# Optimization experiments

Measured on AMD Instinct MI355X. Metric: run time of the kernel, lower is better.

Reference implementation:

```python
import jax, jax.numpy as jnp
import numpy as np
from jax.scipy.special import erf

# module constants (init kwargs)
BOX = 128
RES = 1.0
EPS_IN = 6.5
EPS_OUT = 79.0
ION_SIZE = 1.0
WAT_SIZE = 1.4
ASIGMA = 2.0
KAPPA02 = 0.106
CHARGE_CONV = 7046.52
WR = 8       # splat window radius in voxels ~ ceil(R_max + probe + d*asigma)
N_ITER = 30  # Jacobi iterations for the linearized PB solve


def setup_inputs():
    key = jax.random.key(0)
    kc, kq, kr, kn = jax.random.split(key, 4)
    B, N = 2, 1024
    lo, hi = 0.2 * BOX * RES, 0.8 * BOX * RES
    coords = jax.random.uniform(kc, (B, 3 * N), dtype=jnp.float32, minval=lo, maxval=hi)
    charges = 0.5 * jax.random.normal(kq, (B, N), dtype=jnp.float32)
    radii = jax.random.uniform(kr, (B, N), dtype=jnp.float32, minval=1.0, maxval=2.0)
    assigned_params = jnp.stack([charges, radii], axis=-1)  # [B,N,2] = (charge, radius)
    num_atoms = jax.random.randint(kn, (B,), N // 2, N + 1, dtype=jnp.int32)
    return {"coords": coords, "assigned_params": assigned_params, "num_atoms": num_atoms}


def _flat_scatter_add(vals, idx, B):
    # idx [...,3] int32 clipped voxel indices; vals same leading shape; batched scatter-add
    flat = (idx[..., 0] * BOX + idx[..., 1]) * BOX + idx[..., 2]
    flat = flat + (jnp.arange(B, dtype=jnp.int32) * (BOX ** 3)).reshape((B,) + (1,) * (flat.ndim - 1))
    acc = jnp.zeros((B * BOX ** 3,), vals.dtype).at[flat.reshape(-1)].add(vals.reshape(-1))
    return acc.reshape(B, BOX, BOX, BOX)


def _eps_channel(xyz, radii, atom_mask, offset, extra_r):
    # rho_sum(x) = prod_atoms (1 - smoothed_indicator); accumulated in log space via scatter-add
    o = jnp.arange(-WR, WR + 1, dtype=jnp.int32)
    offs = jnp.stack(jnp.meshgrid(o, o, o, indexing="ij"), axis=-1).reshape(-1, 3)  # [W3,3]
    idx0 = jnp.round(xyz / RES - offset).astype(jnp.int32)            # [B,N,3]
    idx = idx0[:, :, None, :] + offs[None, None]                      # [B,N,W3,3]
    pos = (idx.astype(xyz.dtype) + offset) * RES
    r = jnp.sqrt(jnp.sum((pos - xyz[:, :, None, :]) ** 2, axis=-1) + 1e-12)
    rho = 0.5 * (1.0 - erf((r - (radii[:, :, None] + extra_r)) / ASIGMA))
    logv = jnp.log1p(-jnp.clip(rho, 0.0, 1.0 - 1e-6))
    inb = jnp.all((idx >= 0) & (idx < BOX), axis=-1)
    logv = jnp.where(inb & atom_mask[:, :, None], logv, 0.0)
    acc = _flat_scatter_add(logv, jnp.clip(idx, 0, BOX - 1), xyz.shape[0])
    return jnp.exp(acc)


def _coords2q(xyz, charges, atom_mask):
    # trilinear charge spreading onto the voxel grid
    g = xyz / RES
    i0 = jnp.floor(g).astype(jnp.int32)
    f = g - i0.astype(g.dtype)
    c = jnp.stack(jnp.meshgrid(*([jnp.arange(2)] * 3), indexing="ij"), -1).reshape(-1, 3)  # [8,3]
    idx = i0[:, :, None, :] + c[None, None]                           # [B,N,8,3]
    w = jnp.prod(jnp.where(c[None, None].astype(bool), f[:, :, None, :], 1.0 - f[:, :, None, :]), axis=-1)
    vals = w * charges[:, :, None]
    inb = jnp.all((idx >= 0) & (idx < BOX), axis=-1)
    vals = jnp.where(inb & atom_mask[:, :, None], vals, 0.0)
    return _flat_scatter_add(vals, jnp.clip(idx, 0, BOX - 1), xyz.shape[0])


def _shift(a, axis, step):
    # out[i] = a[i+step], zero padded (Dirichlet phi=0 boundary)
    pad = [(0, 0)] * a.ndim
    sl = [slice(None)] * a.ndim
    if step == 1:
        pad[axis] = (0, 1); sl[axis] = slice(1, None)
    else:
        pad[axis] = (1, 0); sl[axis] = slice(0, -1)
    return jnp.pad(a, pad)[tuple(sl)]


def _qeps2phi(q, eps):
    # Jacobi iteration for div(eps grad phi) - kappa02*lambda*phi = -q on staggered eps grids
    ex, ey, ez, lmbd = eps[:, 0], eps[:, 1], eps[:, 2], eps[:, 3]
    exm, eym, ezm = _shift(ex, 1, -1), _shift(ey, 2, -1), _shift(ez, 3, -1)
    denom = ex + exm + ey + eym + ez + ezm + KAPPA02 * lmbd * RES ** 2
    rhs = q * RES ** 2
    def body(_, phi):
        num = (ex * _shift(phi, 1, 1) + exm * _shift(phi, 1, -1)
               + ey * _shift(phi, 2, 1) + eym * _shift(phi, 2, -1)
               + ez * _shift(phi, 3, 1) + ezm * _shift(phi, 3, -1) + rhs)
        return num / denom
    return jax.lax.fori_loop(0, N_ITER, body, jnp.zeros_like(q))


def reference(coords, assigned_params, num_atoms):
    B = coords.shape[0]
    N = coords.shape[1] // 3
    xyz = coords.reshape(B, N, 3)
    atom_mask = jnp.arange(N)[None, :] < num_atoms[:, None]
    charges, radii = assigned_params[..., 0], assigned_params[..., 1]
    # channels 0..2: face-staggered eps grids (water probe); channel 3: ion accessibility
    specs = [((0.5, 0.0, 0.0), WAT_SIZE), ((0.0, 0.5, 0.0), WAT_SIZE),
             ((0.0, 0.0, 0.5), WAT_SIZE), ((0.0, 0.0, 0.0), ION_SIZE)]
    rho = jnp.stack([_eps_channel(xyz, radii, atom_mask, jnp.asarray(off, xyz.dtype), er)
                     for off, er in specs], axis=1)  # [B,4,S,S,S]
    eps = jnp.concatenate([(1.0 - rho[:, :3]) * (EPS_IN - EPS_OUT) + EPS_OUT,
                           (1.0 - rho[:, 3:4])], axis=1)
    q = _coords2q(xyz, charges, atom_mask) * CHARGE_CONV
    phi = _qeps2phi(q, eps)
    return (q, eps, phi)
```

## Files before the change

### kernel.cpp

```cpp
#include <hip/hip_runtime.h>
#include <math.h>

#define BOX 128
#define MCELLS (BOX*BOX*BOX)
#define TABN 512
#define SATN 256
typedef unsigned short u16;

__device__ __forceinline__ float bf2f(u16 h) {
  union { unsigned u; float f; } c; c.u = ((unsigned)h) << 16; return c.f;
}
__device__ __forceinline__ u16 f2bf(float f) {
  union { float f; unsigned u; } c; c.f = f;
  unsigned r = c.u + 0x7FFF + ((c.u >> 16) & 1);
  return (u16)(r >> 16);
}
__device__ __forceinline__ unsigned pk2(float a, float b) {
  return (unsigned)f2bf(a) | ((unsigned)f2bf(b) << 16);
}
__device__ __forceinline__ float plo(unsigned p) {
  union { unsigned u; float f; } c; c.u = p << 16; return c.f;
}
__device__ __forceinline__ float phh(unsigned p) {
  union { unsigned u; float f; } c; c.u = p & 0xFFFF0000u; return c.f;
}
__device__ __forceinline__ void up8(uint4 p, float* o) {
  o[0] = plo(p.x); o[1] = phh(p.x); o[2] = plo(p.y); o[3] = phh(p.y);
  o[4] = plo(p.z); o[5] = phh(p.z); o[6] = plo(p.w); o[7] = phh(p.w);
}
__device__ __forceinline__ uint4 pk8(const float* o) {
  return make_uint4(pk2(o[0], o[1]), pk2(o[2], o[3]),
                    pk2(o[4], o[5]), pk2(o[6], o[7]));
}

__device__ __forceinline__ float f_exact(float u) {
  float au = fabsf(u);
  float tt = __builtin_amdgcn_rcpf(fmaf(0.3275911f, au, 1.0f));
  float poly = tt * fmaf(tt, fmaf(tt, fmaf(tt, fmaf(tt, 1.061405429f,
                   -1.453152027f), 1.421413741f), -0.284496736f),
                   0.254829592f);
  float e = fmaf(-poly, __expf(-u * u), 1.0f);
  float erfu = (u < 0.0f) ? -e : e;
  float s = fmaf(0.5f, erfu, 0.5f);
  s = fminf(fmaxf(s, 1e-6f), 1.0f);
  return __logf(s);
}

__device__ __forceinline__ float tlookf(const float2* __restrict__ ftab,
                                        float r2, float aoff, float hidu) {
  float r = __builtin_amdgcn_sqrtf(r2);
  float t = fmaf(r, hidu, aoff);
  t = fminf(fmaxf(t, 0.0f), 511.75f);
  int j = (int)t;
  float fr = t - (float)j;
  float2 e = ftab[j];
  return fmaf(fr, e.y, e.x);
}

__global__ __launch_bounds__(256) void eps_gather_kernel(
    const float* __restrict__ coords, const float* __restrict__ params,
    const int* __restrict__ num_atoms, float* __restrict__ eps_out, int N) {
  __shared__ float4 satA[SATN];
  __shared__ float  satW[SATN];
  __shared__ float2 ftab[TABN];
  __shared__ int scnt;

  const int xt = blockIdx.x, yt = blockIdx.y;
  const int bz = blockIdx.z;
  const int b = bz >> 4, zt = bz & 15;
  const int tid = threadIdx.x;

  const float u0 = -1.8f;
  const float du = (2.2f - u0) / (float)TABN;
  const float inv_du = (float)TABN / (2.2f - u0);
  const float hidu = 0.5f * inv_du;
  const float dAI = 0.2f * inv_du;

  if (tid == 0) scnt = 0;
  __syncthreads();

  const float lox = (float)(xt * 8), hix = lox + 7.5f;
  const float loy = (float)(yt * 8), hiy = loy + 7.5f;
  const float loz = (float)(zt * 8), hiz = loz + 7.5f;

  const int na = num_atoms[b];
  for (int a = tid; a < N; a += 256) {
    if (a < na) {
      float ax = coords[(size_t)b * 3 * N + a * 3 + 0];
      float ay = coords[(size_t)b * 3 * N + a * 3 + 1];
      float az = coords[(size_t)b * 3 * N + a * 3 + 2];
      float rad = params[((size_t)b * N + a) * 2 + 1];
      float cx = fminf(fmaxf(ax, lox), hix);
      float cy = fminf(fmaxf(ay, loy), hiy);
      float cz = fminf(fmaxf(az, loz), hiz);
      float ddx = ax - cx, ddy = ay - cy, ddz = az - cz;
      float cut = rad + 5.85f;
      if (ddx * ddx + ddy * ddy + ddz * ddz < cut * cut) {
        int s = atomicAdd(&scnt, 1);
        if (s < SATN) {
          float Rw = rad + 1.4f;
          float cw = rad + 5.8f;
          satA[s] = make_float4(ax, ay, az, cw * cw);
          satW[s] = (1.8f - 0.5f * Rw) * inv_du;
        }
      }
    }
  }
  __syncthreads();
  const int cnt = min(scnt, SATN);

  const int zq = tid & 3, yy = (tid >> 2) & 7, xx = tid >> 5;
  const int xi = xt * 8 + xx, yi = yt * 8 + yy, zi = zt * 8 + zq * 2;
  const int v = (xi << 14) + (yi << 7) + zi;
  const size_t eb = (size_t)b * 4 * MCELLS;

  if (cnt == 0) {
    *(float2*)(eps_out + eb + 0 * MCELLS + v) = make_float2(79.0f, 79.0f);
    *(float2*)(eps_out + eb + 1 * MCELLS + v) = make_float2(79.0f, 79.0f);
    *(float2*)(eps_out + eb + 2 * MCELLS + v) = make_float2(79.0f, 79.0f);
    *(float2*)(eps_out + eb + (size_t)3 * MCELLS + v) = make_float2(0.0f, 0.0f);
    return;
  }

  for (int j = tid; j < TABN; j += 256) {
    float uj = fmaf(du, (float)j, u0);
    float f0 = f_exact(uj);
    float f1 = f_exact(uj + du);
    ftab[j] = (j == TABN - 1) ? make_float2(0.0f, 0.0f)
                              : make_float2(f0, f1 - f0);
  }
  __syncthreads();

  const float xf = (float)xi, yf = (float)yi, zf = (float)zi;
  float acc[4][2] = {{0.f, 0.f}, {0.f, 0.f}, {0.f, 0.f}, {0.f, 0.f}};

  for (int j = 0; j < cnt; ++j) {
    float4 A = satA[j];
    float aW = satW[j];
    float dx = xf - A.x, dy = yf - A.y, dzb = zf - A.z;
    float cw2 = A.w;

    float dx2 = dx * dx, dxh = dx + 0.5f, dxh2 = dxh * dxh;
    float dy2 = dy * dy, dyh = dy + 0.5f, dyh2 = dyh * dyh;
    float mdx = fminf(dx2, dxh2);
    float mdy = fminf(dy2, dyh2);
    float zhi = dzb + 1.5f;
    float mdz = (dzb > 0.f) ? dzb * dzb : (zhi < 0.f ? zhi * zhi : 0.f);
    if (mdx + mdy + mdz >= cw2) continue;

    float aI = aW + dAI;
    float sW0 = dxh2 + dy2, sW1 = dx2 + dyh2, sxy = dx2 + dy2;
#pragma unroll
    for (int k = 0; k < 2; ++k) {
      float dzv = dzb + (float)k;
      float dz2 = dzv * dzv, dzh = dzv + 0.5f, dzh2 = dzh * dzh;
      acc[0][k] += tlookf(ftab, sW0 + dz2, aW, hidu);
      acc[1][k] += tlookf(ftab, sW1 + dz2, aW, hidu);
      acc[2][k] += tlookf(ftab, sxy + dzh2, aW, hidu);
      acc[3][k] += tlookf(ftab, sxy + dz2, aI, hidu);
    }
  }

#pragma unroll
  for (int ch = 0; ch < 4; ++ch) {
    float e0 = __expf(acc[ch][0]), e1 = __expf(acc[ch][1]);
    float2 o = (ch < 3)
        ? make_float2(fmaf(72.5f, e0, 6.5f), fmaf(72.5f, e1, 6.5f))
        : make_float2(1.0f - e0, 1.0f - e1);
    *(float2*)(eps_out + eb + (size_t)ch * MCELLS + v) = o;
  }
}

__global__ __launch_bounds__(256) void q_scatter_kernel(
    const float* __restrict__ coords, const float* __restrict__ params,
    const int* __restrict__ num_atoms, float* __restrict__ q, int N, int B) {
  int t = blockIdx.x * blockDim.x + threadIdx.x;
  if (t >= B * N) return;
  int b = t / N, atom = t % N;
  if (atom >= num_atoms[b]) return;

  const float x = coords[(size_t)b * 3 * N + atom * 3 + 0];
  const float y = coords[(size_t)b * 3 * N + atom * 3 + 1];
  const float z = coords[(size_t)b * 3 * N + atom * 3 + 2];
  const float c = params[((size_t)b * N + atom) * 2 + 0] * 7046.52f;

  float fx0 = floorf(x), fy0 = floorf(y), fz0 = floorf(z);
  int ix = (int)fx0, iy = (int)fy0, iz = (int)fz0;
  float fx = x - fx0, fy = y - fy0, fz = z - fz0;

  float* __restrict__ g = q + (size_t)b * MCELLS;
  for (int k = 0; k < 8; ++k) {
    int cx = (k >> 2) & 1, cy = (k >> 1) & 1, cz = k & 1;
    int jx = ix + cx, jy = iy + cy, jz = iz + cz;
    if ((unsigned)jx >= (unsigned)BOX || (unsigned)jy >= (unsigned)BOX ||
        (unsigned)jz >= (unsigned)BOX) continue;
    float w = (cx ? fx : 1.0f - fx) * (cy ? fy : 1.0f - fy) *
              (cz ? fz : 1.0f - fz);
    atomicAdd(&g[(jx * BOX + jy) * BOX + jz], w * c);
  }
}

__global__ __launch_bounds__(256) void prep8_kernel(
    const float* __restrict__ eps, const float* __restrict__ q,
    u16* __restrict__ exb, u16* __restrict__ eyb, u16* __restrict__ ezb,
    u16* __restrict__ rdn, u16* __restrict__ rq2, u16* __restrict__ phiA,
    u16* __restrict__ pure16, int B) {
  const int per_b = MCELLS / 8;
  int t = blockIdx.x * 256 + threadIdx.x;
  if (t >= B * per_b) return;
  int b = t >> 18;
  int r = t & (per_b - 1);
  int zg = r & 15, y = (r >> 4) & 127, x = r >> 11;
  int z0 = zg << 3;
  int v = (x << 14) | (y << 7) | z0;
  size_t cell = (size_t)b * MCELLS + v;

  const float* ex = eps + (size_t)(b * 4 + 0) * MCELLS;
  const float* ey = eps + (size_t)(b * 4 + 1) * MCELLS;
  const float* ez = eps + (size_t)(b * 4 + 2) * MCELLS;
  const float* lm = eps + (size_t)(b * 4 + 3) * MCELLS;

  float exA[8], eyA[8], ezA9[9], lA[8], qA[8], xmA[8], ymA[8];
  *(float4*)(exA)     = *(const float4*)(ex + v);
  *(float4*)(exA + 4) = *(const float4*)(ex + v + 4);
  *(float4*)(eyA)     = *(const float4*)(ey + v);
  *(float4*)(eyA + 4) = *(const float4*)(ey + v + 4);
  *(float4*)(ezA9 + 1) = *(const float4*)(ez + v);
  *(float4*)(ezA9 + 5) = *(const float4*)(ez + v + 4);
  ezA9[0] = (z0 > 0) ? ez[v - 1] : 0.0f;
  *(float4*)(lA)     = *(const float4*)(lm + v);
  *(float4*)(lA + 4) = *(const float4*)(lm + v + 4);
  *(float4*)(qA)     = *(const float4*)(q + cell);
  *(float4*)(qA + 4) = *(const float4*)(q + cell + 4);
  if (x > 0) {
    *(float4*)(xmA)     = *(const float4*)(ex + v - 16384);
    *(float4*)(xmA + 4) = *(const float4*)(ex + v - 16384 + 4);
  } else {
#pragma unroll
    for (int i = 0; i < 8; ++i) xmA[i] = 0.0f;
  }
  if (y > 0) {
    *(float4*)(ymA)     = *(const float4*)(ey + v - 128);
    *(float4*)(ymA + 4) = *(const float4*)(ey + v - 128 + 4);
  } else {
#pragma unroll
    for (int i = 0; i < 8; ++i) ymA[i] = 0.0f;
  }

  float rdA[8], rqA[8];
  bool pu = true;
#pragma unroll
  for (int i = 0; i < 8; ++i) {
    float den = exA[i] + xmA[i] + eyA[i] + ymA[i] + ezA9[i + 1] + ezA9[i] +
                0.106f * lA[i];
    rdA[i] = __builtin_amdgcn_rcpf(den);
    rqA[i] = qA[i] * rdA[i];
    pu &= (exA[i] == 79.0f) & (eyA[i] == 79.0f) & (ezA9[i + 1] == 79.0f) &
          (lA[i] == 0.0f) & (qA[i] == 0.0f);
  }
  *(uint4*)(exb + cell) = pk8(exA);
  *(uint4*)(eyb + cell) = pk8(eyA);
  *(uint4*)(ezb + cell) = pk8(ezA9 + 1);
  *(uint4*)(rdn + cell) = pk8(rdA);
  uint4 rqp = pk8(rqA);
  *(uint4*)(rq2 + cell) = rqp;
  *(uint4*)(phiA + cell) = rqp;

  unsigned long long bal = __ballot(pu);
  int lane = threadIdx.x & 63;
  if ((lane & 15) == 0) {
    unsigned m = (unsigned)((bal >> (lane & 48)) & 0xFFFFull);
    pure16[((size_t)b << 14) + (x << 7) + y] = (u16)m;
  }
}

__global__ __launch_bounds__(256) void flag_kernel(
    const u16* __restrict__ pure16, unsigned char* __restrict__ flags,
    int B) {
  int t = blockIdx.x * 256 + threadIdx.x;
  if (t >= B * 128 * 32) return;
  int b = t >> 12;
  int r = t & 4095;
  int x = r >> 5, yq = r & 31;
  unsigned char f = 0;
  if (x > 0 && x < 127 && yq > 0 && yq < 31) {
    const u16* P = pure16 + ((size_t)b << 14);
    bool ok = true;
    int y0 = yq << 2;
    for (int dx = -1; dx <= 1; ++dx)
      for (int yy = y0 - 1; yy <= y0 + 4; ++yy)
        ok &= (P[(x + dx) * 128 + yy] == 0xFFFFu);
    f = ok ? 1 : 0;
  }
  flags[t] = f;
}

__device__ __forceinline__ void stage8(
    const u16* __restrict__ sp, int cst, int c0, int z0, size_t cell,
    int gx, int gy, bool bulk,
    const u16* __restrict__ exb, const u16* __restrict__ eyb,
    const u16* __restrict__ ezb, const u16* __restrict__ rdn,
    const u16* __restrict__ rq2, float* o) {
  const u16* pc0 = sp + (c0 << 7) + z0;
  uint4 pc = *(const uint4*)pc0;
  u16 zmu = (z0 > 0)   ? pc0[-1] : (u16)0;
  u16 zpu = (z0 < 120) ? pc0[8]  : (u16)0;
  uint4 xp = *(const uint4*)(pc0 + (cst << 7));
  uint4 xm = *(const uint4*)(pc0 - (cst << 7));
  uint4 yp = *(const uint4*)(pc0 + 128);
  uint4 ym = *(const uint4*)(pc0 - 128);

  float pz[10];
  pz[0] = bf2f(zmu); up8(pc, pz + 1); pz[9] = bf2f(zpu);
  float xpA[8], xmA[8], ypA[8], ymA[8];
  up8(xp, xpA); up8(xm, xmA); up8(yp, ypA); up8(ym, ymA);

  if (bulk) {
    float rdc  = bf2f(f2bf(__builtin_amdgcn_rcpf(474.0f)));
    float rdc0 = bf2f(f2bf(__builtin_amdgcn_rcpf(395.0f)));
#pragma unroll
    for (int i = 0; i < 8; ++i) {
      float s = xpA[i] + xmA[i] + ypA[i] + ymA[i] + pz[i] + pz[i + 2];
      float rd = (z0 + i == 0) ? rdc0 : rdc;
      o[i] = rd * (79.0f * s);
    }
  } else {
    const uint4 z4 = make_uint4(0, 0, 0, 0);
    uint4 ec  = *(const uint4*)(exb + cell);
    uint4 em  = (gx > 0) ? *(const uint4*)(exb + cell - 16384) : z4;
    uint4 yc  = *(const uint4*)(eyb + cell);
    uint4 ym4 = (gy > 0) ? *(const uint4*)(eyb + cell - 128) : z4;
    uint4 zc  = *(const uint4*)(ezb + cell);
    u16 ezm0  = (z0 > 0) ? ezb[cell - 1] : (u16)0;
    uint4 rd4 = *(const uint4*)(rdn + cell);
    uint4 rq4 = *(const uint4*)(rq2 + cell);
    float exA[8], exmA[8], eyA[8], eymA[8], ezA[9], rdA[8], rqA[8];
    up8(ec, exA); up8(em, exmA); up8(yc, eyA); up8(ym4, eymA);
    ezA[0] = bf2f(ezm0); up8(zc, ezA + 1);
    up8(rd4, rdA); up8(rq4, rqA);
#pragma unroll
    for (int i = 0; i < 8; ++i) {
      float num = exA[i] * xpA[i];
      num = fmaf(exmA[i], xmA[i], num);
      num = fmaf(eyA[i],  ypA[i], num);
      num = fmaf(eymA[i], ymA[i], num);
      num = fmaf(ezA[i + 1], pz[i + 2], num);
      num = fmaf(ezA[i],     pz[i],     num);
      o[i] = fmaf(rdA[i], num, rqA[i]);
    }
  }
}

__global__ __launch_bounds__(256, 4) void fused2_kernel(
    const u16* __restrict__ pin, u16* __restrict__ pout,
    const u16* __restrict__ exb, const u16* __restrict__ eyb,
    const u16* __restrict__ ezb, const u16* __restrict__ rdn,
    const u16* __restrict__ rq2, const u16* __restrict__ pure16) {
  __shared__ u16 s0[12 * 8 * 128];
  __shared__ u16 s1[10 * 6 * 128];
  __shared__ u16 sbulk16[96];

  const int flat = blockIdx.x;
  const int xcd = flat & 7;
  const int idx = flat >> 3;
  const int x0 = ((xcd << 1) | (idx & 1)) * 8;
  const int rem = idx >> 1;
  const int y0 = (rem & 31) * 4;
  const int b = rem >> 5;

  const int tid = threadIdx.x;
  const size_t bbase = (size_t)b << 21;
  const uint4 z4 = make_uint4(0, 0, 0, 0);

  if (tid < 96) {
    int cx = tid >> 3, cy = tid & 7;
    int gx = x0 - 2 + cx, gy = y0 - 2 + cy;
    unsigned sb = 0;
    if (gx >= 1 && gx <= 126 && gy >= 1 && gy <= 126) {
      const u16* P = pure16 + ((size_t)b << 14);
      sb = (unsigned)P[(gx << 7) + gy] & P[((gx - 1) << 7) + gy] &
           P[((gx + 1) << 7) + gy] & P[(gx << 7) + gy - 1] &
           P[(gx << 7) + gy + 1];
    }
    sbulk16[tid] = (u16)(sb & ((sb << 1) | 1u));
  }

  for (int i = tid; i < 96 * 16; i += 256) {
    int col = i >> 4, zc = i & 15;
    int cx = col >> 3, cy = col & 7;
    int gx = x0 - 2 + cx, gy = y0 - 2 + cy;
    uint4 vv = z4;
    if ((unsigned)gx < 128u && (unsigned)gy < 128u)
      vv = *(const uint4*)(pin + (bbase | (gx << 14) | (gy << 7) | (zc << 3)));
    ((uint4*)s0)[(col << 4) + zc] = vv;
  }
  __syncthreads();

  for (int u = tid; u < 60 * 16; u += 256) {
    int col = u >> 4, zc = u & 15, zz = zc << 3;
    int cx = col / 6, cy = col - cx * 6;
    int gx = x0 - 1 + cx, gy = y0 - 1 + cy;
    uint4* dst = (uint4*)(s1 + (col << 7) + zz);
    if ((unsigned)gx >= 128u || (unsigned)gy >= 128u) { *dst = z4; continue; }
    int c0 = (cx + 1) * 8 + (cy + 1);
    size_t cell = bbase | (gx << 14) | (gy << 7) | zz;
    float o[8];
    stage8(s0, 8, c0, zz, cell, gx, gy, ((sbulk16[c0] >> zc) & 1) != 0,
           exb, eyb, ezb, rdn, rq2, o);
    *dst = pk8(o);
  }
  __syncthreads();

  for (int u = tid; u < 32 * 16; u += 256) {
    int col = u >> 4, zc = u & 15, zz = zc << 3;
    int cx = col >> 2, cy = col & 3;
    int gx = x0 + cx, gy = y0 + cy;
    int c1 = (cx + 1) * 6 + (cy + 1);
    size_t cell = bbase | (gx << 14) | (gy << 7) | zz;
    float o[8];
    stage8(s1, 6, c1, zz, cell, gx, gy,
           ((sbulk16[(cx + 2) * 8 + (cy + 2)] >> zc) & 1) != 0,
           exb, eyb, ezb, rdn, rq2, o);
    *(uint4*)(pout + cell) = pk8(o);
  }
}

__global__ __launch_bounds__(256) void sweep_final_kernel(
    const u16* __restrict__ pin, float* __restrict__ poutf,
    const u16* __restrict__ exb, const u16* __restrict__ eyb,
    const u16* __restrict__ ezb, const u16* __restrict__ rdn,
    const u16* __restrict__ rq2, const unsigned char* __restrict__ flags,
    int units) {
  int t = blockIdx.x * 256 + threadIdx.x;
  if (t >= units) return;
  int b = t >> 18;
  int r = t & ((1 << 18) - 1);
  int zg = r & 15, y = (r >> 4) & 127, x = r >> 11;
  int z0 = zg << 3;
  int v = (x << 14) | (y << 7) | z0;
  size_t cell = (size_t)b * MCELLS + v;

  const uint4 z4 = make_uint4(0, 0, 0, 0);
  uint4 pc = *(const uint4*)(pin + cell);
  u16 zmu = (z0 > 0)   ? pin[cell - 1] : (u16)0;
  u16 zpu = (z0 < 120) ? pin[cell + 8] : (u16)0;
  uint4 xp = (x < 127) ? *(const uint4*)(pin + cell + 16384) : z4;
  uint4 xm = (x > 0)   ? *(const uint4*)(pin + cell - 16384) : z4;
  uint4 yp = (y < 127) ? *(const uint4*)(pin + cell + 128) : z4;
  uint4 ym = (y > 0)   ? *(const uint4*)(pin + cell - 128) : z4;

  float pz[10];
  pz[0] = bf2f(zmu); up8(pc, pz + 1); pz[9] = bf2f(zpu);
  float xpA[8], xmA[8], ypA[8], ymA[8];
  up8(xp, xpA); up8(xm, xmA); up8(yp, ypA); up8(ym, ymA);

  bool bulk = flags[(b << 12) + (x << 5) + (y >> 2)] != 0;

  float o[8];
  if (bulk) {
    float rdc  = bf2f(f2bf(__builtin_amdgcn_rcpf(474.0f)));
    float rdc0 = bf2f(f2bf(__builtin_amdgcn_rcpf(395.0f)));
#pragma unroll
    for (int i = 0; i < 8; ++i) {
      float s = xpA[i] + xmA[i] + ypA[i] + ymA[i] + pz[i] + pz[i + 2];
      float rd = (z0 + i == 0) ? rdc0 : rdc;
      o[i] = rd * (79.0f * s);
    }
  } else {
    uint4 ec  = *(const uint4*)(exb + cell);
    uint4 em  = (x > 0) ? *(const uint4*)(exb + cell - 16384) : z4;
    uint4 yc  = *(const uint4*)(eyb + cell);
    uint4 ym4 = (y > 0) ? *(const uint4*)(eyb + cell - 128) : z4;
    uint4 zc  = *(const uint4*)(ezb + cell);
    u16 ezm0  = (z0 > 0) ? ezb[cell - 1] : (u16)0;
    uint4 rd4 = *(const uint4*)(rdn + cell);
    uint4 rq4 = *(const uint4*)(rq2 + cell);
    float exA[8], exmA[8], eyA[8], eymA[8], ezA[9], rdA[8], rqA[8];
    up8(ec, exA); up8(em, exmA); up8(yc, eyA); up8(ym4, eymA);
    ezA[0] = bf2f(ezm0); up8(zc, ezA + 1);
    up8(rd4, rdA); up8(rq4, rqA);
#pragma unroll
    for (int i = 0; i < 8; ++i) {
      float num = exA[i] * xpA[i];
      num = fmaf(exmA[i], xmA[i], num);
      num = fmaf(eyA[i],  ypA[i], num);
      num = fmaf(eymA[i], ymA[i], num);
      num = fmaf(ezA[i + 1], pz[i + 2], num);
      num = fmaf(ezA[i],     pz[i],     num);
      o[i] = fmaf(rdA[i], num, rqA[i]);
    }
  }
  *(float4*)(poutf + cell)     = make_float4(o[0], o[1], o[2], o[3]);
  *(float4*)(poutf + cell + 4) = make_float4(o[4], o[5], o[6], o[7]);
}

__global__ __launch_bounds__(256) void jacobi_kernel(
    const float* __restrict__ phi_in, float* __restrict__ phi_out,
    const float* __restrict__ eps, const float* __restrict__ rhs, int B) {
  int i = blockIdx.x * blockDim.x + threadIdx.x;
  if (i >= B * MCELLS) return;
  int b = i >> 21;
  int v = i & (MCELLS - 1);
  int z = v & 127, y = (v >> 7) & 127, x = v >> 14;

  const float* ex = eps + (size_t)(b * 4 + 0) * MCELLS;
  const float* ey = eps + (size_t)(b * 4 + 1) * MCELLS;
  const float* ez = eps + (size_t)(b * 4 + 2) * MCELLS;
  const float* lm = eps + (size_t)(b * 4 + 3) * MCELLS;
  const float* p  = phi_in + (size_t)b * MCELLS;

  float exc = ex[v], eyc = ey[v], ezc = ez[v];
  float exm = (x > 0) ? ex[v - BOX * BOX] : 0.0f;
  float eym = (y > 0) ? ey[v - BOX]       : 0.0f;
  float ezm = (z > 0) ? ez[v - 1]         : 0.0f;

  float num = rhs[i];
  num += (x < BOX - 1) ? exc * p[v + BOX * BOX] : 0.0f;
  num += (x > 0)       ? exm * p[v - BOX * BOX] : 0.0f;
  num += (y < BOX - 1) ? eyc * p[v + BOX]       : 0.0f;
  num += (y > 0)       ? eym * p[v - BOX]       : 0.0f;
  num += (z < BOX - 1) ? ezc * p[v + 1]         : 0.0f;
  num += (z > 0)       ? ezm * p[v - 1]         : 0.0f;

  float den = exc + exm + eyc + eym + ezc + ezm + 0.106f * lm[v];
  phi_out[i] = num / den;
}

extern "C" void kernel_launch(void* const* d_in, const int* in_sizes, int n_in,
                              void* d_out, int out_size, void* d_ws,
                              size_t ws_size, hipStream_t stream) {
  const float* coords    = (const float*)d_in[0];
  const float* params    = (const float*)d_in[1];
  const int*   num_atoms = (const int*)d_in[2];

  const int B = in_sizes[2];
  const int N = in_sizes[1] / (2 * B);

  float* out = (float*)d_out;
  float* q   = out;
  float* eps = out + (size_t)B * MCELLS;
  float* phi = out + (size_t)B * MCELLS * 5;

  const size_t BM = (size_t)B * MCELLS;
  u16* phiA = (u16*)d_ws;
  u16* phiB = phiA + BM;
  u16* exb  = phiB + BM;
  u16* eyb  = exb + BM;
  u16* ezb  = eyb + BM;
  u16* rdn  = ezb + BM;
  u16* rq2  = rdn + BM;
  u16* pure16 = rq2 + BM;
  unsigned char* flags = (unsigned char*)(pure16 + (size_t)B * 16384);
  const size_t need = BM * 14 + (size_t)B * (32768 + 4096);

  const bool fast = (ws_size >= need);

  hipMemsetAsync(q, 0, sizeof(float) * BM, stream);

  eps_gather_kernel<<<dim3(16, 16, 16 * B), 256, 0, stream>>>(
      coords, params, num_atoms, eps, N);
  q_scatter_kernel<<<(B * N + 255) / 256, 256, 0, stream>>>(
      coords, params, num_atoms, q, N, B);

  if (fast) {
    const int pblocks = B * 1024;
    prep8_kernel<<<pblocks, 256, 0, stream>>>(eps, q, exb, eyb, ezb, rdn, rq2,
                                              phiA, pure16, B);
    flag_kernel<<<(B * 4096 + 255) / 256, 256, 0, stream>>>(pure16, flags, B);

    u16* pa = phiA;
    u16* pb = phiB;
    for (int k = 0; k < 14; ++k) {
      fused2_kernel<<<512 * B, 256, 0, stream>>>(
          pa, pb, exb, eyb, ezb, rdn, rq2, pure16);
      u16* tmp = pa; pa = pb; pb = tmp;
    }
    const int units = B * (MCELLS / 8);
    sweep_final_kernel<<<(units + 255) / 256, 256, 0, stream>>>(
        pa, phi, exb, eyb, ezb, rdn, rq2, flags, units);
  } else {
    hipMemsetAsync(phi, 0, sizeof(float) * BM, stream);
    float* pa = phi;
    float* pb = (float*)d_ws;
    int total = (int)BM;
    for (int it = 0; it < 30; ++it) {
      jacobi_kernel<<<(total + 255) / 256, 256, 0, stream>>>(pa, pb, eps, q, B);
      float* tmp = pa; pa = pb; pb = tmp;
    }
  }
}
```

Measured before the change: 472.3 us.

## Replace two-step fused shared-memory Jacobi kernel with simple per-iteration sweep kernel

Drops the temporally blocked kernel that did two Jacobi steps per launch through shared memory with halo recomputation. Each iteration now runs as a separate lightweight kernel that reads neighbours directly from global memory, doubling the launch count. This removes the redundant halo work, the shared-memory staging and the block barriers. In exchange it re-reads the grid and coefficients from memory every iteration. The bulk mask now uses only the minus-side neighbour flags.

```diff
diff --git a/kernel.cpp b/kernel.cpp
--- a/kernel.cpp
+++ b/kernel.cpp
@@ -295,26 +295,45 @@
   flags[t] = f;
 }
 
-__device__ __forceinline__ void stage8(
-    const u16* __restrict__ sp, int cst, int c0, int z0, size_t cell,
-    int gx, int gy, bool bulk,
+__global__ __launch_bounds__(256) void sweep8_kernel(
+    const u16* __restrict__ pin, u16* __restrict__ pout,
     const u16* __restrict__ exb, const u16* __restrict__ eyb,
     const u16* __restrict__ ezb, const u16* __restrict__ rdn,
-    const u16* __restrict__ rq2, float* o) {
-  const u16* pc0 = sp + (c0 << 7) + z0;
-  uint4 pc = *(const uint4*)pc0;
-  u16 zmu = (z0 > 0)   ? pc0[-1] : (u16)0;
-  u16 zpu = (z0 < 120) ? pc0[8]  : (u16)0;
-  uint4 xp = *(const uint4*)(pc0 + (cst << 7));
-  uint4 xm = *(const uint4*)(pc0 - (cst << 7));
-  uint4 yp = *(const uint4*)(pc0 + 128);
-  uint4 ym = *(const uint4*)(pc0 - 128);
+    const u16* __restrict__ rq2, const u16* __restrict__ pure16,
+    int units) {
+  int t = blockIdx.x * 256 + threadIdx.x;
+  if (t >= units) return;
+  int b = t >> 18;
+  int r = t & ((1 << 18) - 1);
+  int zg = r & 15, y = (r >> 4) & 127, x = r >> 11;
+  int z0 = zg << 3;
+  int v = (x << 14) | (y << 7) | z0;
+  size_t cell = (size_t)b * MCELLS + v;
+
+  const u16* P = pure16 + ((size_t)b << 14);
+  unsigned m = 0;
+  if (x >= 1 && x <= 126 && y >= 1 && y <= 126) {
+    m = (unsigned)P[(x << 7) + y] & P[((x - 1) << 7) + y] &
+        P[(x << 7) + y - 1];
+    m &= (m << 1) | 1u;
+  }
+  bool bulk = ((m >> zg) & 1) != 0;
+
+  const uint4 z4 = make_uint4(0, 0, 0, 0);
+  uint4 pc = *(const uint4*)(pin + cell);
+  u16 zmu = (z0 > 0)   ? pin[cell - 1] : (u16)0;
+  u16 zpu = (z0 < 120) ? pin[cell + 8] : (u16)0;
+  uint4 xp = (x < 127) ? *(const uint4*)(pin + cell + 16384) : z4;
+  uint4 xm = (x > 0)   ? *(const uint4*)(pin + cell - 16384) : z4;
+  uint4 yp = (y < 127) ? *(const uint4*)(pin + cell + 128) : z4;
+  uint4 ym = (y > 0)   ? *(const uint4*)(pin + cell - 128) : z4;
 
   float pz[10];
   pz[0] = bf2f(zmu); up8(pc, pz + 1); pz[9] = bf2f(zpu);
   float xpA[8], xmA[8], ypA[8], ymA[8];
   up8(xp, xpA); up8(xm, xmA); up8(yp, ypA); up8(ym, ymA);
 
+  float o[8];
   if (bulk) {
     float rdc  = bf2f(f2bf(__builtin_amdgcn_rcpf(474.0f)));
     float rdc0 = bf2f(f2bf(__builtin_amdgcn_rcpf(395.0f)));
@@ -325,11 +344,10 @@
       o[i] = rd * (79.0f * s);
     }
   } else {
-    const uint4 z4 = make_uint4(0, 0, 0, 0);
     uint4 ec  = *(const uint4*)(exb + cell);
-    uint4 em  = (gx > 0) ? *(const uint4*)(exb + cell - 16384) : z4;
+    uint4 em  = (x > 0) ? *(const uint4*)(exb + cell - 16384) : z4;
     uint4 yc  = *(const uint4*)(eyb + cell);
-    uint4 ym4 = (gy > 0) ? *(const uint4*)(eyb + cell - 128) : z4;
+    uint4 ym4 = (y > 0) ? *(const uint4*)(eyb + cell - 128) : z4;
     uint4 zc  = *(const uint4*)(ezb + cell);
     u16 ezm0  = (z0 > 0) ? ezb[cell - 1] : (u16)0;
     uint4 rd4 = *(const uint4*)(rdn + cell);
@@ -349,80 +367,7 @@
       o[i] = fmaf(rdA[i], num, rqA[i]);
     }
   }
-}
-
-__global__ __launch_bounds__(256, 4) void fused2_kernel(
-    const u16* __restrict__ pin, u16* __restrict__ pout,
-    const u16* __restrict__ exb, const u16* __restrict__ eyb,
-    const u16* __restrict__ ezb, const u16* __restrict__ rdn,
-    const u16* __restrict__ rq2, const u16* __restrict__ pure16) {
-  __shared__ u16 s0[12 * 8 * 128];
-  __shared__ u16 s1[10 * 6 * 128];
-  __shared__ u16 sbulk16[96];
-
-  const int flat = blockIdx.x;
-  const int xcd = flat & 7;
-  const int idx = flat >> 3;
-  const int x0 = ((xcd << 1) | (idx & 1)) * 8;
-  const int rem = idx >> 1;
-  const int y0 = (rem & 31) * 4;
-  const int b = rem >> 5;
-
-  const int tid = threadIdx.x;
-  const size_t bbase = (size_t)b << 21;
-  const uint4 z4 = make_uint4(0, 0, 0, 0);
-
-  if (tid < 96) {
-    int cx = tid >> 3, cy = tid & 7;
-    int gx = x0 - 2 + cx, gy = y0 - 2 + cy;
-    unsigned sb = 0;
-    if (gx >= 1 && gx <= 126 && gy >= 1 && gy <= 126) {
-      const u16* P = pure16 + ((size_t)b << 14);
-      sb = (unsigned)P[(gx << 7) + gy] & P[((gx - 1) << 7) + gy] &
-           P[((gx + 1) << 7) + gy] & P[(gx << 7) + gy - 1] &
-           P[(gx << 7) + gy + 1];
-    }
-    sbulk16[tid] = (u16)(sb & ((sb << 1) | 1u));
-  }
-
-  for (int i = tid; i < 96 * 16; i += 256) {
-    int col = i >> 4, zc = i & 15;
-    int cx = col >> 3, cy = col & 7;
-    int gx = x0 - 2 + cx, gy = y0 - 2 + cy;
-    uint4 vv = z4;
-    if ((unsigned)gx < 128u && (unsigned)gy < 128u)
-      vv = *(const uint4*)(pin + (bbase | (gx << 14) | (gy << 7) | (zc << 3)));
-    ((uint4*)s0)[(col << 4) + zc] = vv;
-  }
-  __syncthreads();
-
-  for (int u = tid; u < 60 * 16; u += 256) {
-    int col = u >> 4, zc = u & 15, zz = zc << 3;
-    int cx = col / 6, cy = col - cx * 6;
-    int gx = x0 - 1 + cx, gy = y0 - 1 + cy;
-    uint4* dst = (uint4*)(s1 + (col << 7) + zz);
-    if ((unsigned)gx >= 128u || (unsigned)gy >= 128u) { *dst = z4; continue; }
-    int c0 = (cx + 1) * 8 + (cy + 1);
-    size_t cell = bbase | (gx << 14) | (gy << 7) | zz;
-    float o[8];
-    stage8(s0, 8, c0, zz, cell, gx, gy, ((sbulk16[c0] >> zc) & 1) != 0,
-           exb, eyb, ezb, rdn, rq2, o);
-    *dst = pk8(o);
-  }
-  __syncthreads();
-
-  for (int u = tid; u < 32 * 16; u += 256) {
-    int col = u >> 4, zc = u & 15, zz = zc << 3;
-    int cx = col >> 2, cy = col & 3;
-    int gx = x0 + cx, gy = y0 + cy;
-    int c1 = (cx + 1) * 6 + (cy + 1);
-    size_t cell = bbase | (gx << 14) | (gy << 7) | zz;
-    float o[8];
-    stage8(s1, 6, c1, zz, cell, gx, gy,
-           ((sbulk16[(cx + 2) * 8 + (cy + 2)] >> zc) & 1) != 0,
-           exb, eyb, ezb, rdn, rq2, o);
-    *(uint4*)(pout + cell) = pk8(o);
-  }
+  *(uint4*)(pout + cell) = pk8(o);
 }
 
 __global__ __launch_bounds__(256) void sweep_final_kernel(
@@ -568,16 +513,16 @@
                                               phiA, pure16, B);
     flag_kernel<<<(B * 4096 + 255) / 256, 256, 0, stream>>>(pure16, flags, B);
 
+    const int units8 = B * (MCELLS / 8);
     u16* pa = phiA;
     u16* pb = phiB;
-    for (int k = 0; k < 14; ++k) {
-      fused2_kernel<<<512 * B, 256, 0, stream>>>(
-          pa, pb, exb, eyb, ezb, rdn, rq2, pure16);
+    for (int k = 0; k < 28; ++k) {
+      sweep8_kernel<<<(units8 + 255) / 256, 256, 0, stream>>>(
+          pa, pb, exb, eyb, ezb, rdn, rq2, pure16, units8);
       u16* tmp = pa; pa = pb; pb = tmp;
     }
-    const int units = B * (MCELLS / 8);
-    sweep_final_kernel<<<(units + 255) / 256, 256, 0, stream>>>(
-        pa, phi, exb, eyb, ezb, rdn, rq2, flags, units);
+    sweep_final_kernel<<<(units8 + 255) / 256, 256, 0, stream>>>(
+        pa, phi, exb, eyb, ezb, rdn, rq2, flags, units8);
   } else {
     hipMemsetAsync(phi, 0, sizeof(float) * BM, stream);
     float* pa = phi;
```

Result: slower. 675.1 us (+42.9%).
